# Optimization experiments

Measured on AMD Instinct MI355X. Metric: run time of the kernel, lower is better.

## Reference

```python
import jax, jax.numpy as jnp
import numpy as np

B, N, C, H = 2, 2304, 1280, 8   # batch (uncond+cond), tokens (48x48 latent), inner dim, heads
DH = C // H                      # 160, matches the judge shape [16, 256, 160]
SCALE = 1.0 / (DH ** 0.5)
NEG = -1e4                       # additive isolation-mask value


def setup_inputs() -> dict:
    key = jax.random.key(0)
    k0, k1, k2, k3, k4 = jax.random.split(key, 5)
    hidden_states = jax.random.normal(k0, (B, N, C), jnp.float32)
    W_q = jax.random.normal(k1, (C, C), jnp.float32) * 0.02
    W_k = jax.random.normal(k2, (C, C), jnp.float32) * 0.02
    W_v = jax.random.normal(k3, (C, C), jnp.float32) * 0.02
    # broadcast over heads, mirroring _hide_other_subjects_from_subjects output
    vis = jax.random.uniform(k4, (B, 1, N, N)) < 0.9
    masks = jnp.where(vis, 0.0, NEG).astype(jnp.float32)
    return {"hidden_states": hidden_states, "W_q": W_q, "W_k": W_k, "W_v": W_v, "masks": masks}


def _head_to_batch(x):
    # [B, N, C] -> [B*H, N, DH]  (attn.head_to_batch_dim)
    return x.reshape(B, N, H, DH).transpose(0, 2, 1, 3).reshape(B * H, N, DH)


def reference(hidden_states, W_q, W_k, W_v, masks):
    # projections (weights stored pre-transposed so y = x @ W)
    q = _head_to_batch(hidden_states @ W_q)
    k = _head_to_batch(hidden_states @ W_k)
    v = _head_to_batch(hidden_states @ W_v)
    # use_ba self-attention branch: recomputed QK^T + isolation mask + softmax + bmm
    sim = jnp.einsum('bid,bjd->bij', q, k) * SCALE          # [B*H, N, N]
    sim = sim.reshape(B, H, N, N) + masks                   # broadcast mask over heads
    attn = jax.nn.softmax(sim, axis=-1).reshape(B * H, N, N)
    out = jnp.einsum('bij,bjd->bid', attn, v)               # [B*H, N, DH]
    # rearrange '(b h) n d -> b n (h d)'
    return out.reshape(B, H, N, DH).transpose(0, 2, 1, 3).reshape(B, N, H * DH)
```

## Files before the change

### kernel.cpp

```cpp
#include <hip/hip_runtime.h>

#define N_TOK 2304
#define CDIM  1280
#define NH    8
#define DH    160
#define NKT   36
#define SCALE 0.07905694150420949f
#define LOG2E 1.4426950408889634f

#define FRAG_BH   737280
#define KCH_STR   10240
#define VCH_STR   5120

typedef __attribute__((ext_vector_type(8))) short bf16x8;
typedef __attribute__((ext_vector_type(4))) float f32x4;
typedef __attribute__((ext_vector_type(16))) float f32x16;

#define MFMA16(a, b, c) __builtin_amdgcn_mfma_f32_16x16x32_bf16((a), (b), (c), 0, 0, 0)
#define MFMA32(a, b, c) __builtin_amdgcn_mfma_f32_32x32x16_bf16((a), (b), (c), 0, 0, 0)

static __device__ __forceinline__ unsigned short f2bf(float f) {
  unsigned int u = __builtin_bit_cast(unsigned int, f);
  u += 0x7fffu + ((u >> 16) & 1u);
  return (unsigned short)(u >> 16);
}

static __device__ __forceinline__ float fexp2(float x) {
#if __has_builtin(__builtin_amdgcn_exp2f)
  return __builtin_amdgcn_exp2f(x);
#else
  return exp2f(x);
#endif
}

static __device__ __forceinline__ void gload_lds16(const void* g, void* l) {
  const __attribute__((address_space(1))) unsigned int* gp =
      (const __attribute__((address_space(1))) unsigned int*)(unsigned long long)(uintptr_t)g;
  __attribute__((address_space(3))) unsigned int* lp =
      (__attribute__((address_space(3))) unsigned int*)(unsigned int)(uintptr_t)l;
  __builtin_amdgcn_global_load_lds(gp, lp, 16, 0, 0);
}


__global__ void cast_x_kernel(const float* __restrict__ x, unsigned short* __restrict__ xbf) {
  int i = blockIdx.x * 256 + threadIdx.x;
  const float4* p = (const float4*)x + (size_t)i * 2;
  float4 a = p[0], b = p[1];
  union { unsigned short u[8]; uint4 v; } pk;
  pk.u[0] = f2bf(a.x); pk.u[1] = f2bf(a.y); pk.u[2] = f2bf(a.z); pk.u[3] = f2bf(a.w);
  pk.u[4] = f2bf(b.x); pk.u[5] = f2bf(b.y); pk.u[6] = f2bf(b.z); pk.u[7] = f2bf(b.w);
  ((uint4*)xbf)[i] = pk.v;
}

__global__ void transpose_w_kernel(const float* __restrict__ wq, const float* __restrict__ wk,
                                   const float* __restrict__ wv, unsigned short* __restrict__ wt) {
  __shared__ float t[32][33];
  const int w = blockIdx.z;
  const float* src = (w == 0) ? wq : ((w == 1) ? wk : wv);
  const int bx = blockIdx.x * 32;
  const int by = blockIdx.y * 32;
  const int tx = threadIdx.x, ty = threadIdx.y;
  for (int i = 0; i < 32; i += 8)
    t[ty + i][tx] = src[(size_t)(by + ty + i) * CDIM + bx + tx];
  __syncthreads();
  for (int i = 0; i < 32; i += 8)
    wt[((size_t)w * CDIM + bx + ty + i) * CDIM + by + tx] = f2bf(t[tx][ty + i]);
}

__global__ void mask_bits_kernel(const float* __restrict__ masks,
                                 unsigned int* __restrict__ bitsF) {
  int t = blockIdx.x * 256 + threadIdx.x;
  int word = t >> 6, lane = t & 63;
  int jblk = word % NKT, bi = word / NKT;
  float m = masks[(size_t)bi * N_TOK + jblk * 64 + lane];
  unsigned long long vis = __ballot(m > -5000.0f);
  int b = bi / N_TOK, i = bi - b * N_TOK;
  int qt = i >> 5, ql = i & 31;
  unsigned base = ((unsigned)(b * 72 + qt) * 72 + 2 * jblk) * 32 + ql;
  if (lane == 0)      bitsF[base]      = (unsigned)vis;
  else if (lane == 1) bitsF[base + 32] = (unsigned)(vis >> 32);
}

__global__ __launch_bounds__(256, 3) void gemm_qkv_kernel(
    const unsigned short* __restrict__ xbf, const unsigned short* __restrict__ wt,
    char* __restrict__ qfrag, char* __restrict__ kfrag, char* __restrict__ vfrag) {
  __shared__ unsigned short Al[128][64];
  __shared__ unsigned short Bl[128][64];
  const int tid = threadIdx.x;
  const int lane = tid & 63, wv = tid >> 6;
  const int wm = wv >> 1, wn = wv & 1;
  const int l15 = lane & 15, l4 = lane >> 4;
  const int m0 = blockIdx.x * 128, n0 = blockIdx.y * 128;
  const int lr8 = lane >> 3;
  const int scb = ((lane & 7) * 16) ^ (lr8 << 4);
  f32x4 zero = {0.f, 0.f, 0.f, 0.f};
  f32x4 acc[4][4];
#pragma unroll
  for (int mt = 0; mt < 4; mt++)
#pragma unroll
    for (int nt = 0; nt < 4; nt++) acc[mt][nt] = zero;

  for (int kk = 0; kk < CDIM; kk += 64) {
    __syncthreads();
    {
      const char* asrc = (const char*)&xbf[(size_t)(m0 + wv * 32) * CDIM + kk];
      const char* bsrc = (const char*)&wt [(size_t)(n0 + wv * 32) * CDIM + kk];
#pragma unroll
      for (int i = 0; i < 4; i++) {
        gload_lds16(asrc + (size_t)(i * 8 + lr8) * (CDIM * 2) + scb, &Al[wv * 32 + i * 8][0]);
        gload_lds16(bsrc + (size_t)(i * 8 + lr8) * (CDIM * 2) + scb, &Bl[wv * 32 + i * 8][0]);
      }
    }
    __syncthreads();
#pragma unroll
    for (int ks = 0; ks < 2; ks++) {
      bf16x8 af[4], bfr[4];
#pragma unroll
      for (int mt = 0; mt < 4; mt++) {
        int rA = wm * 64 + mt * 16 + l15;
        af[mt] = *(const bf16x8*)((const char*)Al + rA * 128 +
                                  ((ks * 64 + l4 * 16) ^ ((rA & 7) << 4)));
      }
#pragma unroll
      for (int nt = 0; nt < 4; nt++) {
        int rB = wn * 64 + nt * 16 + l15;
        bfr[nt] = *(const bf16x8*)((const char*)Bl + rB * 128 +
                                   ((ks * 64 + l4 * 16) ^ ((rB & 7) << 4)));
      }
#pragma unroll
      for (int mt = 0; mt < 4; mt++)
#pragma unroll
        for (int nt = 0; nt < 4; nt++)
          acc[mt][nt] = MFMA16(af[mt], bfr[nt], acc[mt][nt]);
    }
  }

  const int w_idx = n0 / CDIM;
  if (w_idx == 0) {
    const float qsc = (float)(0.07905694150420949 * 1.4426950408889634);
#pragma unroll
    for (int mt = 0; mt < 4; mt++)
#pragma unroll
      for (int nt = 0; nt < 4; nt++) acc[mt][nt] *= qsc;
  }
  const int cbase = n0 - w_idx * CDIM + wn * 64;
#pragma unroll
  for (int mt = 0; mt < 4; mt++) {
    const int mg = m0 + wm * 64 + mt * 16 + l4 * 4;
    const int b = mg / N_TOK;
    const int tok = mg - b * N_TOK;
#pragma unroll
    for (int nt = 0; nt < 4; nt++) {
      const int cw = cbase + nt * 16 + l15;
      const int h = cw / DH, d = cw - h * DH;
      const size_t bh = (size_t)(b * NH + h);
      if (w_idx == 2) {
        union { unsigned short u[4]; unsigned long long v; } pk;
        pk.u[0] = f2bf(acc[mt][nt][0]); pk.u[1] = f2bf(acc[mt][nt][1]);
        pk.u[2] = f2bf(acc[mt][nt][2]); pk.u[3] = f2bf(acc[mt][nt][3]);
        char* p = vfrag + bh * FRAG_BH + (tok >> 4) * VCH_STR + (d >> 5) * 1024
                  + ((d & 31) + 32 * ((tok >> 3) & 1)) * 16 + (tok & 7) * 2;
        *(unsigned long long*)p = pk.v;
      } else {
        char* base = (w_idx == 0 ? qfrag : kfrag) + bh * FRAG_BH + (d >> 4) * 1024
                     + ((d >> 3) & 1) * 512 + (d & 7) * 2;
#pragma unroll
        for (int r = 0; r < 4; r++) {
          int t2 = tok + r;
          *(unsigned short*)(base + (t2 >> 5) * KCH_STR + (t2 & 31) * 16) =
              f2bf(acc[mt][nt][r]);
        }
      }
    }
  }
}

__global__ __launch_bounds__(64, 2) void attn8_kernel(
    const char* __restrict__ qfrag, const char* __restrict__ kfrag,
    const char* __restrict__ vfrag, const unsigned int* __restrict__ bitsF,
    float* __restrict__ out) {
  __shared__ __align__(16) char smem[20480];
  const int lane = threadIdx.x & 63;
  const int l31 = lane & 31, h = lane >> 5;
  const int lane16 = lane * 16;
  const int id = blockIdx.x;
  const int rem = (id & 7) * 144 + (id >> 3);
  const int bh = rem / 72, qt = rem - (rem / 72) * 72;
  const int b = bh >> 3;
  const int q0 = qt * 32;

  const char* qfb = qfrag + (size_t)bh * FRAG_BH + (size_t)qt * KCH_STR;
  const char* kfb = kfrag + (size_t)bh * FRAG_BH;
  const char* vfb = vfrag + (size_t)bh * FRAG_BH;
  const unsigned int* bb = bitsF + (size_t)(b * 72 + qt) * 72 * 32 + l31;

  bf16x8 qf[10];
#pragma unroll
  for (int ks = 0; ks < 10; ks++) qf[ks] = *(const bf16x8*)(qfb + ks * 1024 + lane16);

  const f32x16 zz = {0.f,0.f,0.f,0.f,0.f,0.f,0.f,0.f,0.f,0.f,0.f,0.f,0.f,0.f,0.f,0.f};
  f32x16 o[5];
#pragma unroll
  for (int dt = 0; dt < 5; dt++) o[dt] = zz;
  float run_m = -3.0e38f, run_l = 0.0f;

  bf16x8 kf[10];
#pragma unroll
  for (int ks = 0; ks < 10; ks++) kf[ks] = *(const bf16x8*)(kfb + ks * 1024 + lane16);

  for (int kt = 0; kt < 72; kt++) {
    unsigned mw = bb[kt * 32];

    const char* vch = vfb + (size_t)kt * KCH_STR;
    bf16x8 va[5], vb_[5];
#pragma unroll
    for (int dt = 0; dt < 5; dt++) va[dt] = *(const bf16x8*)(vch + dt * 1024 + lane16);
#pragma unroll
    for (int dt = 0; dt < 5; dt++)
      vb_[dt] = *(const bf16x8*)(vch + 5120 + dt * 1024 + lane16);

    f32x16 s = zz;
    __builtin_amdgcn_s_setprio(1);
#pragma unroll
    for (int ks = 0; ks < 10; ks++) s = MFMA32(kf[ks], qf[ks], s);
    __builtin_amdgcn_s_setprio(0);

    if (kt + 1 < 72) {
      const char* kr = kfb + (size_t)(kt + 1) * KCH_STR;
#pragma unroll
      for (int ks = 0; ks < 10; ks++) kf[ks] = *(const bf16x8*)(kr + ks * 1024 + lane16);
    }

    float t0 = fmaxf(fmaxf(fmaxf(s[0], s[1]), fmaxf(s[2], s[3])),
                     fmaxf(fmaxf(s[4], s[5]), fmaxf(s[6], s[7])));
    float t1 = fmaxf(fmaxf(fmaxf(s[8], s[9]), fmaxf(s[10], s[11])),
                     fmaxf(fmaxf(s[12], s[13]), fmaxf(s[14], s[15])));
    float pm = fmaxf(t0, t1);
    pm = fmaxf(pm, __shfl_xor(pm, 32));

    if (!__all(pm - run_m <= 8.0f)) {
      float nm = fmaxf(run_m, pm);
      float f = fexp2(run_m - nm);
      run_m = nm;
      run_l *= f;
#pragma unroll
      for (int dt = 0; dt < 5; dt++) o[dt] *= f;
    }

    float rs = 0.0f;
    unsigned pw[8];
#pragma unroll
    for (int i = 0; i < 8; i++) {
      int k0 = ((2 * i) & 3) + 8 * (i >> 1) + 4 * h;
      float p0 = fexp2(s[2 * i] - run_m);
      float p1 = fexp2(s[2 * i + 1] - run_m);
      p0 = ((mw >> k0) & 1u) ? p0 : 0.0f;
      p1 = ((mw >> (k0 + 1)) & 1u) ? p1 : 0.0f;
      rs += p0 + p1;
      unsigned w;
      asm("v_cvt_pk_bf16_f32 %0, %1, %2" : "=v"(w) : "v"(p0), "v"(p1));
      pw[i] = w;
    }
    rs += __shfl_xor(rs, 32);
    run_l += rs;

    {
      unsigned a1 = pw[0], b1 = pw[2];
      asm("v_permlane32_swap_b32 %0, %1" : "+v"(a1), "+v"(b1));
      unsigned a2 = pw[1], b2 = pw[3];
      asm("v_permlane32_swap_b32 %0, %1" : "+v"(a2), "+v"(b2));
      union { unsigned w[4]; bf16x8 v; } u;
      u.w[0] = a1; u.w[1] = a2; u.w[2] = b1; u.w[3] = b2;
      __builtin_amdgcn_s_setprio(1);
#pragma unroll
      for (int dt = 0; dt < 5; dt++) o[dt] = MFMA32(va[dt], u.v, o[dt]);
      __builtin_amdgcn_s_setprio(0);
      unsigned c1 = pw[4], d1 = pw[6];
      asm("v_permlane32_swap_b32 %0, %1" : "+v"(c1), "+v"(d1));
      unsigned c2 = pw[5], d2 = pw[7];
      asm("v_permlane32_swap_b32 %0, %1" : "+v"(c2), "+v"(d2));
      union { unsigned w[4]; bf16x8 v; } u2;
      u2.w[0] = c1; u2.w[1] = c2; u2.w[2] = d1; u2.w[3] = d2;
      __builtin_amdgcn_s_setprio(1);
#pragma unroll
      for (int dt = 0; dt < 5; dt++) o[dt] = MFMA32(vb_[dt], u2.v, o[dt]);
      __builtin_amdgcn_s_setprio(0);
    }
  }

  float invl = 1.0f / run_l;
#pragma unroll
  for (int dt = 0; dt < 5; dt++)
#pragma unroll
    for (int rr = 0; rr < 4; rr++) {
      float4 t;
      t.x = o[dt][4 * rr + 0] * invl;
      t.y = o[dt][4 * rr + 1] * invl;
      t.z = o[dt][4 * rr + 2] * invl;
      t.w = o[dt][4 * rr + 3] * invl;
      int d0 = dt * 32 + 8 * rr + 4 * h;
      *(float4*)(smem + l31 * 640 + ((d0 * 4) ^ ((l31 & 7) << 4))) = t;
    }
  __syncthreads();
  float* outp = out + ((size_t)b * N_TOK + q0) * CDIM + (bh & 7) * DH;
#pragma unroll
  for (int i = 0; i < 20; i++) {
    int c = i * 64 + lane;
    int q = c / 40, f = c - (c / 40) * 40;
    float4 t = *(const float4*)(smem + q * 640 + ((f * 16) ^ ((q & 7) << 4)));
    *(float4*)&outp[(size_t)q * CDIM + f * 4] = t;
  }
}

extern "C" void kernel_launch(void* const* d_in, const int* in_sizes, int n_in,
                              void* d_out, int out_size, void* d_ws, size_t ws_size,
                              hipStream_t stream) {
  const float* hs    = (const float*)d_in[0];
  const float* wq    = (const float*)d_in[1];
  const float* wk    = (const float*)d_in[2];
  const float* wvw   = (const float*)d_in[3];
  const float* masks = (const float*)d_in[4];
  float* out = (float*)d_out;

  char* ws = (char*)d_ws;
  unsigned short* xbf = (unsigned short*)(ws);
  unsigned short* wt  = (unsigned short*)(ws + 11796480);
  char* qf = ws + 21626880;
  char* kf = ws + 33423360;
  char* vf = ws + 45219840;
  unsigned int* bitsF = (unsigned int*)(ws + 57016320);

  cast_x_kernel<<<2880, 256, 0, stream>>>(hs, xbf);
  transpose_w_kernel<<<dim3(40, 40, 3), dim3(32, 8), 0, stream>>>(wq, wk, wvw, wt);
  mask_bits_kernel<<<41472, 256, 0, stream>>>(masks, bitsF);
  gemm_qkv_kernel<<<dim3(36, 30), 256, 0, stream>>>(xbf, wt, qf, kf, vf);
  attn8_kernel<<<1152, 64, 0, stream>>>(qf, kf, vf, bitsF, out);
}
```

Measured before the change: 187.3 us.

## Share K/V tiles across two query waves via double-buffered LDS staging

Attention blocks now hold two waves that each own a 32-query tile and share one K/V chunk per iteration. The chunk is staged into double-buffered LDS with direct global-to-LDS loads, one wave loading K and the other V. This halves global/L2 reads of K and V and hides load latency behind compute. The cost is a block barrier every iteration, LDS reads in place of direct register loads, and a halved block count with larger LDS use per block.

```diff
diff --git a/kernel.cpp b/kernel.cpp
--- a/kernel.cpp
+++ b/kernel.cpp
@@ -175,18 +175,20 @@
   }
 }
 
-__global__ __launch_bounds__(64, 2) void attn8_kernel(
+__global__ __launch_bounds__(128) void attn9_kernel(
     const char* __restrict__ qfrag, const char* __restrict__ kfrag,
     const char* __restrict__ vfrag, const unsigned int* __restrict__ bitsF,
     float* __restrict__ out) {
-  __shared__ __align__(16) char smem[20480];
-  const int lane = threadIdx.x & 63;
+  __shared__ __align__(16) char smem[40960];
+  const int tid = threadIdx.x;
+  const int lane = tid & 63, wv = tid >> 6;
   const int l31 = lane & 31, h = lane >> 5;
   const int lane16 = lane * 16;
   const int id = blockIdx.x;
-  const int rem = (id & 7) * 144 + (id >> 3);
-  const int bh = rem / 72, qt = rem - (rem / 72) * 72;
+  const int rem = (id & 7) * 72 + (id >> 3);
+  const int bh = rem / 36, qp = rem - (rem / 36) * 36;
   const int b = bh >> 3;
+  const int qt = qp * 2 + wv;
   const int q0 = qt * 32;
 
   const char* qfb = qfrag + (size_t)bh * FRAG_BH + (size_t)qt * KCH_STR;
@@ -204,20 +206,34 @@
   for (int dt = 0; dt < 5; dt++) o[dt] = zz;
   float run_m = -3.0e38f, run_l = 0.0f;
 
-  bf16x8 kf[10];
-#pragma unroll
-  for (int ks = 0; ks < 10; ks++) kf[ks] = *(const bf16x8*)(kfb + ks * 1024 + lane16);
+  auto stage = [&](int t) {
+    char* dst = smem + (t & 1) * 20480;
+    if (wv == 0) {
+      const char* ksrc = kfb + (size_t)t * KCH_STR;
+#pragma unroll
+      for (int i = 0; i < 10; i++)
+        gload_lds16(ksrc + i * 1024 + lane16, dst + i * 1024);
+    } else {
+      const char* vsrc = vfb + (size_t)t * KCH_STR;
+#pragma unroll
+      for (int i = 0; i < 10; i++)
+        gload_lds16(vsrc + i * 1024 + lane16, dst + 10240 + i * 1024);
+    }
+  };
+
+  stage(0);
 
   for (int kt = 0; kt < 72; kt++) {
+    __syncthreads();
+    if (kt + 1 < 72) stage(kt + 1);
+    const char* kl = smem + (kt & 1) * 20480;
+    const char* vl = kl + 10240;
+
     unsigned mw = bb[kt * 32];
 
-    const char* vch = vfb + (size_t)kt * KCH_STR;
-    bf16x8 va[5], vb_[5];
-#pragma unroll
-    for (int dt = 0; dt < 5; dt++) va[dt] = *(const bf16x8*)(vch + dt * 1024 + lane16);
-#pragma unroll
-    for (int dt = 0; dt < 5; dt++)
-      vb_[dt] = *(const bf16x8*)(vch + 5120 + dt * 1024 + lane16);
+    bf16x8 kf[10];
+#pragma unroll
+    for (int ks = 0; ks < 10; ks++) kf[ks] = *(const bf16x8*)(kl + ks * 1024 + lane16);
 
     f32x16 s = zz;
     __builtin_amdgcn_s_setprio(1);
@@ -225,11 +241,12 @@
     for (int ks = 0; ks < 10; ks++) s = MFMA32(kf[ks], qf[ks], s);
     __builtin_amdgcn_s_setprio(0);
 
-    if (kt + 1 < 72) {
-      const char* kr = kfb + (size_t)(kt + 1) * KCH_STR;
-#pragma unroll
-      for (int ks = 0; ks < 10; ks++) kf[ks] = *(const bf16x8*)(kr + ks * 1024 + lane16);
-    }
+    bf16x8 va[5], vb_[5];
+#pragma unroll
+    for (int dt = 0; dt < 5; dt++) va[dt] = *(const bf16x8*)(vl + dt * 1024 + lane16);
+#pragma unroll
+    for (int dt = 0; dt < 5; dt++)
+      vb_[dt] = *(const bf16x8*)(vl + 5120 + dt * 1024 + lane16);
 
     float t0 = fmaxf(fmaxf(fmaxf(s[0], s[1]), fmaxf(s[2], s[3])),
                      fmaxf(fmaxf(s[4], s[5]), fmaxf(s[6], s[7])));
@@ -288,6 +305,8 @@
     }
   }
 
+  __syncthreads();
+  char* ob = smem + wv * 20480;
   float invl = 1.0f / run_l;
 #pragma unroll
   for (int dt = 0; dt < 5; dt++)
@@ -299,7 +318,7 @@
       t.z = o[dt][4 * rr + 2] * invl;
       t.w = o[dt][4 * rr + 3] * invl;
       int d0 = dt * 32 + 8 * rr + 4 * h;
-      *(float4*)(smem + l31 * 640 + ((d0 * 4) ^ ((l31 & 7) << 4))) = t;
+      *(float4*)(ob + l31 * 640 + ((d0 * 4) ^ ((l31 & 7) << 4))) = t;
     }
   __syncthreads();
   float* outp = out + ((size_t)b * N_TOK + q0) * CDIM + (bh & 7) * DH;
@@ -307,7 +326,7 @@
   for (int i = 0; i < 20; i++) {
     int c = i * 64 + lane;
     int q = c / 40, f = c - (c / 40) * 40;
-    float4 t = *(const float4*)(smem + q * 640 + ((f * 16) ^ ((q & 7) << 4)));
+    float4 t = *(const float4*)(ob + q * 640 + ((f * 16) ^ ((q & 7) << 4)));
     *(float4*)&outp[(size_t)q * CDIM + f * 4] = t;
   }
 }
@@ -334,5 +353,5 @@
   transpose_w_kernel<<<dim3(40, 40, 3), dim3(32, 8), 0, stream>>>(wq, wk, wvw, wt);
   mask_bits_kernel<<<41472, 256, 0, stream>>>(masks, bitsF);
   gemm_qkv_kernel<<<dim3(36, 30), 256, 0, stream>>>(xbf, wt, qf, kf, vf);
-  attn8_kernel<<<1152, 64, 0, stream>>>(qf, kf, vf, bitsF, out);
-}
+  attn9_kernel<<<576, 128, 0, stream>>>(qf, kf, vf, bitsF, out);
+}
```

After: 246.8 us. 31.8% more time.

## Process two query tiles per attention wave and fuse prep kernels

Applied to the files above, without the earlier changes.

The attention kernel now handles two 32-row query tiles per single-wave block, so each loaded K and V fragment feeds two tiles of MFMA work. That halves K/V global loads per query. Softmax and PV are factored into helpers, and output is stored per tile with extra barriers. The three preprocessing kernels (x cast, weight transpose, mask bitpacking) are merged into one launch to cut launch overhead. The costs are more VGPRs (launch bounds drop to one block per SIMD) and only 576 blocks, which lowers occupancy and latency hiding on a 256-CU device.

```diff
diff --git a/kernel.cpp b/kernel.cpp
--- a/kernel.cpp
+++ b/kernel.cpp
@@ -41,44 +41,50 @@
   __builtin_amdgcn_global_load_lds(gp, lp, 16, 0, 0);
 }
 
-
-__global__ void cast_x_kernel(const float* __restrict__ x, unsigned short* __restrict__ xbf) {
-  int i = blockIdx.x * 256 + threadIdx.x;
-  const float4* p = (const float4*)x + (size_t)i * 2;
-  float4 a = p[0], b = p[1];
-  union { unsigned short u[8]; uint4 v; } pk;
-  pk.u[0] = f2bf(a.x); pk.u[1] = f2bf(a.y); pk.u[2] = f2bf(a.z); pk.u[3] = f2bf(a.w);
-  pk.u[4] = f2bf(b.x); pk.u[5] = f2bf(b.y); pk.u[6] = f2bf(b.z); pk.u[7] = f2bf(b.w);
-  ((uint4*)xbf)[i] = pk.v;
-}
-
-__global__ void transpose_w_kernel(const float* __restrict__ wq, const float* __restrict__ wk,
-                                   const float* __restrict__ wv, unsigned short* __restrict__ wt) {
-  __shared__ float t[32][33];
-  const int w = blockIdx.z;
-  const float* src = (w == 0) ? wq : ((w == 1) ? wk : wv);
-  const int bx = blockIdx.x * 32;
-  const int by = blockIdx.y * 32;
-  const int tx = threadIdx.x, ty = threadIdx.y;
-  for (int i = 0; i < 32; i += 8)
-    t[ty + i][tx] = src[(size_t)(by + ty + i) * CDIM + bx + tx];
-  __syncthreads();
-  for (int i = 0; i < 32; i += 8)
-    wt[((size_t)w * CDIM + bx + ty + i) * CDIM + by + tx] = f2bf(t[tx][ty + i]);
-}
-
-__global__ void mask_bits_kernel(const float* __restrict__ masks,
-                                 unsigned int* __restrict__ bitsF) {
-  int t = blockIdx.x * 256 + threadIdx.x;
-  int word = t >> 6, lane = t & 63;
-  int jblk = word % NKT, bi = word / NKT;
-  float m = masks[(size_t)bi * N_TOK + jblk * 64 + lane];
-  unsigned long long vis = __ballot(m > -5000.0f);
-  int b = bi / N_TOK, i = bi - b * N_TOK;
-  int qt = i >> 5, ql = i & 31;
-  unsigned base = ((unsigned)(b * 72 + qt) * 72 + 2 * jblk) * 32 + ql;
-  if (lane == 0)      bitsF[base]      = (unsigned)vis;
-  else if (lane == 1) bitsF[base + 32] = (unsigned)(vis >> 32);
+__global__ void prep_fused_kernel(const float* __restrict__ x,
+                                  const float* __restrict__ wq,
+                                  const float* __restrict__ wk,
+                                  const float* __restrict__ wv,
+                                  const float* __restrict__ masks,
+                                  unsigned short* __restrict__ xbf,
+                                  unsigned short* __restrict__ wt,
+                                  unsigned int* __restrict__ bitsF) {
+  const int blk = blockIdx.x;
+  const int tid = threadIdx.x;
+  if (blk < 2880) {
+    int i = blk * 256 + tid;
+    const float4* p = (const float4*)x + (size_t)i * 2;
+    float4 a = p[0], b = p[1];
+    union { unsigned short u[8]; uint4 v; } pk;
+    pk.u[0] = f2bf(a.x); pk.u[1] = f2bf(a.y); pk.u[2] = f2bf(a.z); pk.u[3] = f2bf(a.w);
+    pk.u[4] = f2bf(b.x); pk.u[5] = f2bf(b.y); pk.u[6] = f2bf(b.z); pk.u[7] = f2bf(b.w);
+    ((uint4*)xbf)[i] = pk.v;
+  } else if (blk < 7680) {
+    __shared__ float t[32][33];
+    int idx = blk - 2880;
+    int w = idx / 1600, r = idx - w * 1600;
+    const float* src = (w == 0) ? wq : ((w == 1) ? wk : wv);
+    int bx = (r % 40) * 32, by = (r / 40) * 32;
+    int tx = tid & 31, ty = tid >> 5;
+#pragma unroll
+    for (int i = 0; i < 32; i += 8)
+      t[ty + i][tx] = src[(size_t)(by + ty + i) * CDIM + bx + tx];
+    __syncthreads();
+#pragma unroll
+    for (int i = 0; i < 32; i += 8)
+      wt[((size_t)w * CDIM + bx + ty + i) * CDIM + by + tx] = f2bf(t[tx][ty + i]);
+  } else {
+    int tt = (blk - 7680) * 256 + tid;
+    int word = tt >> 6, lane = tt & 63;
+    int jblk = word % NKT, bi = word / NKT;
+    float m = masks[(size_t)bi * N_TOK + jblk * 64 + lane];
+    unsigned long long vis = __ballot(m > -5000.0f);
+    int b = bi / N_TOK, i = bi - b * N_TOK;
+    int qt = i >> 5, ql = i & 31;
+    unsigned base = ((unsigned)(b * 72 + qt) * 72 + 2 * jblk) * 32 + ql;
+    if (lane == 0)      bitsF[base]      = (unsigned)vis;
+    else if (lane == 1) bitsF[base + 32] = (unsigned)(vis >> 32);
+  }
 }
 
 __global__ __launch_bounds__(256, 3) void gemm_qkv_kernel(
@@ -175,7 +181,69 @@
   }
 }
 
-__global__ __launch_bounds__(64, 2) void attn8_kernel(
+
+static __device__ __forceinline__ void softmax_block(
+    const f32x16& s, unsigned mw, float& run_m, float& run_l,
+    f32x16 (&o)[5], int h, unsigned (&pw)[8]) {
+  float t0 = fmaxf(fmaxf(fmaxf(s[0], s[1]), fmaxf(s[2], s[3])),
+                   fmaxf(fmaxf(s[4], s[5]), fmaxf(s[6], s[7])));
+  float t1 = fmaxf(fmaxf(fmaxf(s[8], s[9]), fmaxf(s[10], s[11])),
+                   fmaxf(fmaxf(s[12], s[13]), fmaxf(s[14], s[15])));
+  float pm = fmaxf(t0, t1);
+  pm = fmaxf(pm, __shfl_xor(pm, 32));
+
+  if (!__all(pm - run_m <= 8.0f)) {
+    float nm = fmaxf(run_m, pm);
+    float f = fexp2(run_m - nm);
+    run_m = nm;
+    run_l *= f;
+#pragma unroll
+    for (int dt = 0; dt < 5; dt++) o[dt] *= f;
+  }
+
+  float rs = 0.0f;
+#pragma unroll
+  for (int i = 0; i < 8; i++) {
+    int k0 = ((2 * i) & 3) + 8 * (i >> 1) + 4 * h;
+    float p0 = fexp2(s[2 * i] - run_m);
+    float p1 = fexp2(s[2 * i + 1] - run_m);
+    p0 = ((mw >> k0) & 1u) ? p0 : 0.0f;
+    p1 = ((mw >> (k0 + 1)) & 1u) ? p1 : 0.0f;
+    rs += p0 + p1;
+    unsigned w;
+    asm("v_cvt_pk_bf16_f32 %0, %1, %2" : "=v"(w) : "v"(p0), "v"(p1));
+    pw[i] = w;
+  }
+  rs += __shfl_xor(rs, 32);
+  run_l += rs;
+}
+
+static __device__ __forceinline__ void pv_block(
+    const unsigned (&pw)[8], const bf16x8 (&va)[5], const bf16x8 (&vb_)[5],
+    f32x16 (&o)[5]) {
+  unsigned a1 = pw[0], b1 = pw[2];
+  asm("v_permlane32_swap_b32 %0, %1" : "+v"(a1), "+v"(b1));
+  unsigned a2 = pw[1], b2 = pw[3];
+  asm("v_permlane32_swap_b32 %0, %1" : "+v"(a2), "+v"(b2));
+  union { unsigned w[4]; bf16x8 v; } u;
+  u.w[0] = a1; u.w[1] = a2; u.w[2] = b1; u.w[3] = b2;
+  __builtin_amdgcn_s_setprio(1);
+#pragma unroll
+  for (int dt = 0; dt < 5; dt++) o[dt] = MFMA32(va[dt], u.v, o[dt]);
+  __builtin_amdgcn_s_setprio(0);
+  unsigned c1 = pw[4], d1 = pw[6];
+  asm("v_permlane32_swap_b32 %0, %1" : "+v"(c1), "+v"(d1));
+  unsigned c2 = pw[5], d2 = pw[7];
+  asm("v_permlane32_swap_b32 %0, %1" : "+v"(c2), "+v"(d2));
+  union { unsigned w[4]; bf16x8 v; } u2;
+  u2.w[0] = c1; u2.w[1] = c2; u2.w[2] = d1; u2.w[3] = d2;
+  __builtin_amdgcn_s_setprio(1);
+#pragma unroll
+  for (int dt = 0; dt < 5; dt++) o[dt] = MFMA32(vb_[dt], u2.v, o[dt]);
+  __builtin_amdgcn_s_setprio(0);
+}
+
+__global__ __launch_bounds__(64, 1) void attn10_kernel(
     const char* __restrict__ qfrag, const char* __restrict__ kfrag,
     const char* __restrict__ vfrag, const unsigned int* __restrict__ bitsF,
     float* __restrict__ out) {
@@ -184,32 +252,37 @@
   const int l31 = lane & 31, h = lane >> 5;
   const int lane16 = lane * 16;
   const int id = blockIdx.x;
-  const int rem = (id & 7) * 144 + (id >> 3);
-  const int bh = rem / 72, qt = rem - (rem / 72) * 72;
+  const int rem = (id & 7) * 72 + (id >> 3);
+  const int bh = rem / 36, qq = rem - (rem / 36) * 36;
   const int b = bh >> 3;
-  const int q0 = qt * 32;
-
-  const char* qfb = qfrag + (size_t)bh * FRAG_BH + (size_t)qt * KCH_STR;
+  const int qt0 = qq * 2;
+
+  const char* qfb0 = qfrag + (size_t)bh * FRAG_BH + (size_t)qt0 * KCH_STR;
   const char* kfb = kfrag + (size_t)bh * FRAG_BH;
   const char* vfb = vfrag + (size_t)bh * FRAG_BH;
-  const unsigned int* bb = bitsF + (size_t)(b * 72 + qt) * 72 * 32 + l31;
-
-  bf16x8 qf[10];
-#pragma unroll
-  for (int ks = 0; ks < 10; ks++) qf[ks] = *(const bf16x8*)(qfb + ks * 1024 + lane16);
+  const unsigned int* bb0 = bitsF + (size_t)(b * 72 + qt0) * 72 * 32 + l31;
+  const unsigned int* bb1 = bb0 + 72 * 32;
+
+  bf16x8 qf0[10], qf1[10];
+#pragma unroll
+  for (int ks = 0; ks < 10; ks++) {
+    qf0[ks] = *(const bf16x8*)(qfb0 + ks * 1024 + lane16);
+    qf1[ks] = *(const bf16x8*)(qfb0 + KCH_STR + ks * 1024 + lane16);
+  }
 
   const f32x16 zz = {0.f,0.f,0.f,0.f,0.f,0.f,0.f,0.f,0.f,0.f,0.f,0.f,0.f,0.f,0.f,0.f};
-  f32x16 o[5];
-#pragma unroll
-  for (int dt = 0; dt < 5; dt++) o[dt] = zz;
-  float run_m = -3.0e38f, run_l = 0.0f;
+  f32x16 o0[5], o1[5];
+#pragma unroll
+  for (int dt = 0; dt < 5; dt++) { o0[dt] = zz; o1[dt] = zz; }
+  float m0 = -3.0e38f, l0 = 0.0f, m1 = -3.0e38f, l1 = 0.0f;
 
   bf16x8 kf[10];
 #pragma unroll
   for (int ks = 0; ks < 10; ks++) kf[ks] = *(const bf16x8*)(kfb + ks * 1024 + lane16);
 
   for (int kt = 0; kt < 72; kt++) {
-    unsigned mw = bb[kt * 32];
+    unsigned mw0 = bb0[kt * 32];
+    unsigned mw1 = bb1[kt * 32];
 
     const char* vch = vfb + (size_t)kt * KCH_STR;
     bf16x8 va[5], vb_[5];
@@ -219,10 +292,12 @@
     for (int dt = 0; dt < 5; dt++)
       vb_[dt] = *(const bf16x8*)(vch + 5120 + dt * 1024 + lane16);
 
-    f32x16 s = zz;
+    f32x16 s0 = zz, s1 = zz;
     __builtin_amdgcn_s_setprio(1);
 #pragma unroll
-    for (int ks = 0; ks < 10; ks++) s = MFMA32(kf[ks], qf[ks], s);
+    for (int ks = 0; ks < 10; ks++) s0 = MFMA32(kf[ks], qf0[ks], s0);
+#pragma unroll
+    for (int ks = 0; ks < 10; ks++) s1 = MFMA32(kf[ks], qf1[ks], s1);
     __builtin_amdgcn_s_setprio(0);
 
     if (kt + 1 < 72) {
@@ -231,85 +306,40 @@
       for (int ks = 0; ks < 10; ks++) kf[ks] = *(const bf16x8*)(kr + ks * 1024 + lane16);
     }
 
-    float t0 = fmaxf(fmaxf(fmaxf(s[0], s[1]), fmaxf(s[2], s[3])),
-                     fmaxf(fmaxf(s[4], s[5]), fmaxf(s[6], s[7])));
-    float t1 = fmaxf(fmaxf(fmaxf(s[8], s[9]), fmaxf(s[10], s[11])),
-                     fmaxf(fmaxf(s[12], s[13]), fmaxf(s[14], s[15])));
-    float pm = fmaxf(t0, t1);
-    pm = fmaxf(pm, __shfl_xor(pm, 32));
-
-    if (!__all(pm - run_m <= 8.0f)) {
-      float nm = fmaxf(run_m, pm);
-      float f = fexp2(run_m - nm);
-      run_m = nm;
-      run_l *= f;
-#pragma unroll
-      for (int dt = 0; dt < 5; dt++) o[dt] *= f;
-    }
-
-    float rs = 0.0f;
-    unsigned pw[8];
-#pragma unroll
-    for (int i = 0; i < 8; i++) {
-      int k0 = ((2 * i) & 3) + 8 * (i >> 1) + 4 * h;
-      float p0 = fexp2(s[2 * i] - run_m);
-      float p1 = fexp2(s[2 * i + 1] - run_m);
-      p0 = ((mw >> k0) & 1u) ? p0 : 0.0f;
-      p1 = ((mw >> (k0 + 1)) & 1u) ? p1 : 0.0f;
-      rs += p0 + p1;
-      unsigned w;
-      asm("v_cvt_pk_bf16_f32 %0, %1, %2" : "=v"(w) : "v"(p0), "v"(p1));
-      pw[i] = w;
-    }
-    rs += __shfl_xor(rs, 32);
-    run_l += rs;
-
-    {
-      unsigned a1 = pw[0], b1 = pw[2];
-      asm("v_permlane32_swap_b32 %0, %1" : "+v"(a1), "+v"(b1));
-      unsigned a2 = pw[1], b2 = pw[3];
-      asm("v_permlane32_swap_b32 %0, %1" : "+v"(a2), "+v"(b2));
-      union { unsigned w[4]; bf16x8 v; } u;
-      u.w[0] = a1; u.w[1] = a2; u.w[2] = b1; u.w[3] = b2;
-      __builtin_amdgcn_s_setprio(1);
-#pragma unroll
-      for (int dt = 0; dt < 5; dt++) o[dt] = MFMA32(va[dt], u.v, o[dt]);
-      __builtin_amdgcn_s_setprio(0);
-      unsigned c1 = pw[4], d1 = pw[6];
-      asm("v_permlane32_swap_b32 %0, %1" : "+v"(c1), "+v"(d1));
-      unsigned c2 = pw[5], d2 = pw[7];
-      asm("v_permlane32_swap_b32 %0, %1" : "+v"(c2), "+v"(d2));
-      union { unsigned w[4]; bf16x8 v; } u2;
-      u2.w[0] = c1; u2.w[1] = c2; u2.w[2] = d1; u2.w[3] = d2;
-      __builtin_amdgcn_s_setprio(1);
-#pragma unroll
-      for (int dt = 0; dt < 5; dt++) o[dt] = MFMA32(vb_[dt], u2.v, o[dt]);
-      __builtin_amdgcn_s_setprio(0);
-    }
-  }
-
-  float invl = 1.0f / run_l;
-#pragma unroll
-  for (int dt = 0; dt < 5; dt++)
-#pragma unroll
-    for (int rr = 0; rr < 4; rr++) {
-      float4 t;
-      t.x = o[dt][4 * rr + 0] * invl;
-      t.y = o[dt][4 * rr + 1] * invl;
-      t.z = o[dt][4 * rr + 2] * invl;
-      t.w = o[dt][4 * rr + 3] * invl;
-      int d0 = dt * 32 + 8 * rr + 4 * h;
-      *(float4*)(smem + l31 * 640 + ((d0 * 4) ^ ((l31 & 7) << 4))) = t;
-    }
-  __syncthreads();
-  float* outp = out + ((size_t)b * N_TOK + q0) * CDIM + (bh & 7) * DH;
-#pragma unroll
-  for (int i = 0; i < 20; i++) {
-    int c = i * 64 + lane;
-    int q = c / 40, f = c - (c / 40) * 40;
-    float4 t = *(const float4*)(smem + q * 640 + ((f * 16) ^ ((q & 7) << 4)));
-    *(float4*)&outp[(size_t)q * CDIM + f * 4] = t;
-  }
+    unsigned pw0[8], pw1[8];
+    softmax_block(s0, mw0, m0, l0, o0, h, pw0);
+    pv_block(pw0, va, vb_, o0);
+    softmax_block(s1, mw1, m1, l1, o1, h, pw1);
+    pv_block(pw1, va, vb_, o1);
+  }
+
+  auto store_tile = [&](const f32x16 (&o)[5], float run_l, int q0v) {
+    float invl = 1.0f / run_l;
+#pragma unroll
+    for (int dt = 0; dt < 5; dt++)
+#pragma unroll
+      for (int rr = 0; rr < 4; rr++) {
+        float4 t;
+        t.x = o[dt][4 * rr + 0] * invl;
+        t.y = o[dt][4 * rr + 1] * invl;
+        t.z = o[dt][4 * rr + 2] * invl;
+        t.w = o[dt][4 * rr + 3] * invl;
+        int d0 = dt * 32 + 8 * rr + 4 * h;
+        *(float4*)(smem + l31 * 640 + ((d0 * 4) ^ ((l31 & 7) << 4))) = t;
+      }
+    __syncthreads();
+    float* outp = out + ((size_t)b * N_TOK + q0v) * CDIM + (bh & 7) * DH;
+#pragma unroll
+    for (int i = 0; i < 20; i++) {
+      int c = i * 64 + lane;
+      int q = c / 40, f = c - (c / 40) * 40;
+      float4 t = *(const float4*)(smem + q * 640 + ((f * 16) ^ ((q & 7) << 4)));
+      *(float4*)&outp[(size_t)q * CDIM + f * 4] = t;
+    }
+    __syncthreads();
+  };
+  store_tile(o0, l0, qt0 * 32);
+  store_tile(o1, l1, qt0 * 32 + 32);
 }
 
 extern "C" void kernel_launch(void* const* d_in, const int* in_sizes, int n_in,
@@ -330,9 +360,7 @@
   char* vf = ws + 45219840;
   unsigned int* bitsF = (unsigned int*)(ws + 57016320);
 
-  cast_x_kernel<<<2880, 256, 0, stream>>>(hs, xbf);
-  transpose_w_kernel<<<dim3(40, 40, 3), dim3(32, 8), 0, stream>>>(wq, wk, wvw, wt);
-  mask_bits_kernel<<<41472, 256, 0, stream>>>(masks, bitsF);
+  prep_fused_kernel<<<49152, 256, 0, stream>>>(hs, wq, wk, wvw, masks, xbf, wt, bitsF);
   gemm_qkv_kernel<<<dim3(36, 30), 256, 0, stream>>>(xbf, wt, qf, kf, vf);
-  attn8_kernel<<<1152, 64, 0, stream>>>(qf, kf, vf, bitsF, out);
-}
+  attn10_kernel<<<576, 64, 0, stream>>>(qf, kf, vf, bitsF, out);
+}
```

New measurement: 332.1 us. 77.3% more time.

## Fuse prep kernels into one launch and pack two query tiles per attention block

Applied to the files above, without the earlier changes.

Three preprocessing kernels (x cast, weight transpose, mask bitpacking) are merged into one kernel that branches on block index, removing two launches and their tail gaps. The attention kernel now runs two waves per block, each handling its own 32-row query tile, with separate LDS staging regions, so half as many blocks are launched. The waves share no K/V data, so the gain is mainly fewer, larger blocks and different occupancy. The fused prep kernel uses 256-thread blocks for the transpose path with LDS declared in one branch, which raises LDS use for every block.

```diff
diff --git a/kernel.cpp b/kernel.cpp
--- a/kernel.cpp
+++ b/kernel.cpp
@@ -41,44 +41,50 @@
   __builtin_amdgcn_global_load_lds(gp, lp, 16, 0, 0);
 }
 
-
-__global__ void cast_x_kernel(const float* __restrict__ x, unsigned short* __restrict__ xbf) {
-  int i = blockIdx.x * 256 + threadIdx.x;
-  const float4* p = (const float4*)x + (size_t)i * 2;
-  float4 a = p[0], b = p[1];
-  union { unsigned short u[8]; uint4 v; } pk;
-  pk.u[0] = f2bf(a.x); pk.u[1] = f2bf(a.y); pk.u[2] = f2bf(a.z); pk.u[3] = f2bf(a.w);
-  pk.u[4] = f2bf(b.x); pk.u[5] = f2bf(b.y); pk.u[6] = f2bf(b.z); pk.u[7] = f2bf(b.w);
-  ((uint4*)xbf)[i] = pk.v;
-}
-
-__global__ void transpose_w_kernel(const float* __restrict__ wq, const float* __restrict__ wk,
-                                   const float* __restrict__ wv, unsigned short* __restrict__ wt) {
-  __shared__ float t[32][33];
-  const int w = blockIdx.z;
-  const float* src = (w == 0) ? wq : ((w == 1) ? wk : wv);
-  const int bx = blockIdx.x * 32;
-  const int by = blockIdx.y * 32;
-  const int tx = threadIdx.x, ty = threadIdx.y;
-  for (int i = 0; i < 32; i += 8)
-    t[ty + i][tx] = src[(size_t)(by + ty + i) * CDIM + bx + tx];
-  __syncthreads();
-  for (int i = 0; i < 32; i += 8)
-    wt[((size_t)w * CDIM + bx + ty + i) * CDIM + by + tx] = f2bf(t[tx][ty + i]);
-}
-
-__global__ void mask_bits_kernel(const float* __restrict__ masks,
-                                 unsigned int* __restrict__ bitsF) {
-  int t = blockIdx.x * 256 + threadIdx.x;
-  int word = t >> 6, lane = t & 63;
-  int jblk = word % NKT, bi = word / NKT;
-  float m = masks[(size_t)bi * N_TOK + jblk * 64 + lane];
-  unsigned long long vis = __ballot(m > -5000.0f);
-  int b = bi / N_TOK, i = bi - b * N_TOK;
-  int qt = i >> 5, ql = i & 31;
-  unsigned base = ((unsigned)(b * 72 + qt) * 72 + 2 * jblk) * 32 + ql;
-  if (lane == 0)      bitsF[base]      = (unsigned)vis;
-  else if (lane == 1) bitsF[base + 32] = (unsigned)(vis >> 32);
+__global__ void prep_fused_kernel(const float* __restrict__ x,
+                                  const float* __restrict__ wq,
+                                  const float* __restrict__ wk,
+                                  const float* __restrict__ wv,
+                                  const float* __restrict__ masks,
+                                  unsigned short* __restrict__ xbf,
+                                  unsigned short* __restrict__ wt,
+                                  unsigned int* __restrict__ bitsF) {
+  const int blk = blockIdx.x;
+  const int tid = threadIdx.x;
+  if (blk < 2880) {
+    int i = blk * 256 + tid;
+    const float4* p = (const float4*)x + (size_t)i * 2;
+    float4 a = p[0], b = p[1];
+    union { unsigned short u[8]; uint4 v; } pk;
+    pk.u[0] = f2bf(a.x); pk.u[1] = f2bf(a.y); pk.u[2] = f2bf(a.z); pk.u[3] = f2bf(a.w);
+    pk.u[4] = f2bf(b.x); pk.u[5] = f2bf(b.y); pk.u[6] = f2bf(b.z); pk.u[7] = f2bf(b.w);
+    ((uint4*)xbf)[i] = pk.v;
+  } else if (blk < 7680) {
+    __shared__ float t[32][33];
+    int idx = blk - 2880;
+    int w = idx / 1600, r = idx - w * 1600;
+    const float* src = (w == 0) ? wq : ((w == 1) ? wk : wv);
+    int bx = (r % 40) * 32, by = (r / 40) * 32;
+    int tx = tid & 31, ty = tid >> 5;
+#pragma unroll
+    for (int i = 0; i < 32; i += 8)
+      t[ty + i][tx] = src[(size_t)(by + ty + i) * CDIM + bx + tx];
+    __syncthreads();
+#pragma unroll
+    for (int i = 0; i < 32; i += 8)
+      wt[((size_t)w * CDIM + bx + ty + i) * CDIM + by + tx] = f2bf(t[tx][ty + i]);
+  } else {
+    int tt = (blk - 7680) * 256 + tid;
+    int word = tt >> 6, lane = tt & 63;
+    int jblk = word % NKT, bi = word / NKT;
+    float m = masks[(size_t)bi * N_TOK + jblk * 64 + lane];
+    unsigned long long vis = __ballot(m > -5000.0f);
+    int b = bi / N_TOK, i = bi - b * N_TOK;
+    int qt = i >> 5, ql = i & 31;
+    unsigned base = ((unsigned)(b * 72 + qt) * 72 + 2 * jblk) * 32 + ql;
+    if (lane == 0)      bitsF[base]      = (unsigned)vis;
+    else if (lane == 1) bitsF[base + 32] = (unsigned)(vis >> 32);
+  }
 }
 
 __global__ __launch_bounds__(256, 3) void gemm_qkv_kernel(
@@ -175,18 +181,20 @@
   }
 }
 
-__global__ __launch_bounds__(64, 2) void attn8_kernel(
+__global__ __launch_bounds__(128, 2) void attn12_kernel(
     const char* __restrict__ qfrag, const char* __restrict__ kfrag,
     const char* __restrict__ vfrag, const unsigned int* __restrict__ bitsF,
     float* __restrict__ out) {
-  __shared__ __align__(16) char smem[20480];
-  const int lane = threadIdx.x & 63;
+  __shared__ __align__(16) char smem[40960];
+  const int tid = threadIdx.x;
+  const int lane = tid & 63, wv = tid >> 6;
   const int l31 = lane & 31, h = lane >> 5;
   const int lane16 = lane * 16;
   const int id = blockIdx.x;
-  const int rem = (id & 7) * 144 + (id >> 3);
-  const int bh = rem / 72, qt = rem - (rem / 72) * 72;
+  const int rem = (id & 7) * 72 + (id >> 3);
+  const int bh = rem / 36, qq = rem - (rem / 36) * 36;
   const int b = bh >> 3;
+  const int qt = qq * 2 + wv;
   const int q0 = qt * 32;
 
   const char* qfb = qfrag + (size_t)bh * FRAG_BH + (size_t)qt * KCH_STR;
@@ -288,6 +296,7 @@
     }
   }
 
+  char* ob = smem + wv * 20480;
   float invl = 1.0f / run_l;
 #pragma unroll
   for (int dt = 0; dt < 5; dt++)
@@ -299,7 +308,7 @@
       t.z = o[dt][4 * rr + 2] * invl;
       t.w = o[dt][4 * rr + 3] * invl;
       int d0 = dt * 32 + 8 * rr + 4 * h;
-      *(float4*)(smem + l31 * 640 + ((d0 * 4) ^ ((l31 & 7) << 4))) = t;
+      *(float4*)(ob + l31 * 640 + ((d0 * 4) ^ ((l31 & 7) << 4))) = t;
     }
   __syncthreads();
   float* outp = out + ((size_t)b * N_TOK + q0) * CDIM + (bh & 7) * DH;
@@ -307,7 +316,7 @@
   for (int i = 0; i < 20; i++) {
     int c = i * 64 + lane;
     int q = c / 40, f = c - (c / 40) * 40;
-    float4 t = *(const float4*)(smem + q * 640 + ((f * 16) ^ ((q & 7) << 4)));
+    float4 t = *(const float4*)(ob + q * 640 + ((f * 16) ^ ((q & 7) << 4)));
     *(float4*)&outp[(size_t)q * CDIM + f * 4] = t;
   }
 }
@@ -330,9 +339,7 @@
   char* vf = ws + 45219840;
   unsigned int* bitsF = (unsigned int*)(ws + 57016320);
 
-  cast_x_kernel<<<2880, 256, 0, stream>>>(hs, xbf);
-  transpose_w_kernel<<<dim3(40, 40, 3), dim3(32, 8), 0, stream>>>(wq, wk, wvw, wt);
-  mask_bits_kernel<<<41472, 256, 0, stream>>>(masks, bitsF);
+  prep_fused_kernel<<<49152, 256, 0, stream>>>(hs, wq, wk, wvw, masks, xbf, wt, bitsF);
   gemm_qkv_kernel<<<dim3(36, 30), 256, 0, stream>>>(xbf, wt, qf, kf, vf);
-  attn8_kernel<<<1152, 64, 0, stream>>>(qf, kf, vf, bitsF, out);
-}
+  attn12_kernel<<<576, 128, 0, stream>>>(qf, kf, vf, bitsF, out);
+}
```

Measured after the change: 189.0 us. Within noise of the previous version (+0.9%).
